# Kernel tuning notes

Hardware: AMD Instinct MI355X
Metric: run time of the kernel (lower is better)

The kernel has to match this reference:

```python
import jax, jax.numpy as jnp
import numpy as np
from jax import lax

B, T, K, HID, NCLS = 32, 2048, 17, 64, 10
DILATIONS = (1, 1, 2)
RESIDUAL = (False, True, True)
TK = 3  # temporal kernel
BN_EPS = 1e-5
LN_EPS = 1e-5

COCO_EDGES = [(0,1),(0,2),(1,3),(2,4),(5,6),(5,7),(7,9),(6,8),(8,10),(5,11),(6,12),(11,13),(13,15),(12,14),(14,16)]

def build_skeleton_adj(num_kpts=K):
    adj = np.eye(num_kpts, dtype=np.float32)
    for i, j in COCO_EDGES:
        adj[i, j] = 1.0
        adj[j, i] = 1.0
    adj = adj + np.eye(num_kpts, dtype=np.float32)
    deg = adj.sum(axis=1, keepdims=True)
    deg[deg == 0] = 1.0
    return adj / deg

def setup_inputs() -> dict:
    key = jax.random.key(0)
    ks = jax.random.split(key, 8)
    kpts = jax.random.normal(ks[0], (B, T, K, 3), dtype=jnp.float32)
    adj = jnp.asarray(build_skeleton_adj(K))
    gcn_w0 = jax.random.normal(ks[1], (3, HID), dtype=jnp.float32) * (1.0 / np.sqrt(3))
    gcn_w1 = jax.random.normal(ks[2], (HID, HID), dtype=jnp.float32) * (1.0 / np.sqrt(HID))
    gcn_w2 = jax.random.normal(ks[3], (HID, HID), dtype=jnp.float32) * (1.0 / np.sqrt(HID))
    tcn_w = jax.random.normal(ks[4], (3, HID, HID, TK, 1), dtype=jnp.float32) * (1.0 / np.sqrt(HID * TK))
    bn_scale = 1.0 + 0.1 * jax.random.normal(ks[5], (3, HID), dtype=jnp.float32)
    bn_bias = 0.1 * jax.random.normal(ks[6], (3, HID), dtype=jnp.float32)
    bn_mean = 0.1 * jax.random.normal(ks[7], (3, HID), dtype=jnp.float32)
    bn_var = 0.5 + jax.random.uniform(jax.random.fold_in(key, 7), (3, HID), dtype=jnp.float32)
    ln_scale = jnp.ones((HID,), dtype=jnp.float32)
    ln_bias = jnp.zeros((HID,), dtype=jnp.float32)
    fc_w = jax.random.normal(jax.random.fold_in(key, 8), (HID, NCLS), dtype=jnp.float32) * (1.0 / np.sqrt(HID))
    fc_b = jnp.zeros((NCLS,), dtype=jnp.float32)
    return dict(kpts=kpts, adj=adj, gcn_w0=gcn_w0, gcn_w1=gcn_w1, gcn_w2=gcn_w2,
                tcn_w=tcn_w, bn_scale=bn_scale, bn_bias=bn_bias, bn_mean=bn_mean,
                bn_var=bn_var, ln_scale=ln_scale, ln_bias=ln_bias, fc_w=fc_w, fc_b=fc_b)

def _stgn_block(x, adj, gw, tw, bs, bb, bm, bv, dilation, residual):
    # x: [B, C_in, T, K]
    y = jnp.einsum('bctk,kv->bctv', x, adj)          # graph conv over keypoints
    y = jnp.einsum('bitk,io->botk', y, gw)           # channel mixing (intended GCN weight)
    pad = (TK - 1) * dilation // 2
    y = lax.conv_general_dilated(y, tw, window_strides=(1, 1),
                                 padding=[(pad, pad), (0, 0)],
                                 rhs_dilation=(dilation, 1),
                                 dimension_numbers=('NCHW', 'OIHW', 'NCHW'))
    inv = (bs / jnp.sqrt(bv + BN_EPS))[None, :, None, None]
    y = y * inv + (bb - bs * bm / jnp.sqrt(bv + BN_EPS))[None, :, None, None]
    y = jax.nn.relu(y)
    if residual:
        y = y + x
    return y

def reference(kpts, adj, gcn_w0, gcn_w1, gcn_w2, tcn_w, bn_scale, bn_bias, bn_mean,
              bn_var, ln_scale, ln_bias, fc_w, fc_b):
    x = jnp.transpose(kpts, (0, 3, 1, 2))  # [B, 3, T, K]
    gws = (gcn_w0, gcn_w1, gcn_w2)
    for i in range(3):
        x = _stgn_block(x, adj, gws[i], tcn_w[i], bn_scale[i], bn_bias[i],
                        bn_mean[i], bn_var[i], DILATIONS[i], RESIDUAL[i])
    feat = x.mean(axis=(2, 3))  # [B, HID] temporal/spatial mean pool
    mu = feat.mean(axis=-1, keepdims=True)
    var = feat.var(axis=-1, keepdims=True)
    feat = (feat - mu) / jnp.sqrt(var + LN_EPS) * ln_scale + ln_bias
    return feat @ fc_w + fc_b  # [B, NCLS]
```

## Files before the change

### kernel.cpp

```cpp
#include <hip/hip_runtime.h>
#include <hip/hip_fp16.h>
#include <math.h>

#define T_DIM 2048
#define TP_DIM 2052
#define K_DIM 17
#define HID   64
#define B_DIM 32

typedef short s16x8 __attribute__((ext_vector_type(8)));
typedef unsigned u32x2 __attribute__((ext_vector_type(2)));
typedef float f32x4 __attribute__((ext_vector_type(4)));
typedef _Float16 f16x2 __attribute__((ext_vector_type(2)));

__device__ __forceinline__ unsigned pkh(float lo, float hi) {
    return __builtin_bit_cast(unsigned, __builtin_amdgcn_cvt_pkrtz(lo, hi));
}
__device__ __forceinline__ f16x2 u2h(unsigned v) {
    return __builtin_bit_cast(f16x2, v);
}
__device__ __forceinline__ unsigned h2u(f16x2 v) {
    return __builtin_bit_cast(unsigned, v);
}
__device__ __forceinline__ short f2h(float f) {
    _Float16 h = (_Float16)f;
    return __builtin_bit_cast(short, h);
}

static constexpr int NBR_PTR[18] = {0,3,6,9,11,13,17,21,24,27,29,31,34,37,40,43,45,47};
static constexpr int NBR_K[47] = {
    0,1,2,  0,1,3,  0,2,4,  1,3,  2,4,
    5,6,7,11,  5,6,8,12,  5,7,9,  6,8,10,  7,9,  8,10,
    5,11,13,  6,12,14,  11,13,15,  12,14,16,  13,15,  14,16 };
__device__ const int d_NBR_PTR[18] = {0,3,6,9,11,13,17,21,24,27,29,31,34,37,40,43,45,47};
__device__ const int d_NBR_K[47] = {
    0,1,2,  0,1,3,  0,2,4,  1,3,  2,4,
    5,6,7,11,  5,6,8,12,  5,7,9,  6,8,10,  7,9,  8,10,
    5,11,13,  6,12,14,  11,13,15,  12,14,16,  13,15,  14,16 };

__global__ void fold_weights_kernel(
    const float* __restrict__ gw0, const float* __restrict__ gw1,
    const float* __restrict__ gw2, const float* __restrict__ tcn,
    const float* __restrict__ bns, const float* __restrict__ bnb,
    const float* __restrict__ bnm, const float* __restrict__ bnv,
    short* __restrict__ effT0, short* __restrict__ effT12,
    float* __restrict__ bnc)
{
    int tid = blockIdx.x * blockDim.x + threadIdx.x;
    int stride = gridDim.x * blockDim.x;
    for (int idx = tid; idx < 2048; idx += stride) {
        int o = idx >> 5, k = idx & 31, dt = k >> 3, cin = k & 7;
        float s = 0.f;
        if (dt < 3 && cin < 3)
            for (int m = 0; m < 64; m++)
                s += gw0[cin * 64 + m] * tcn[(o * 64 + m) * 3 + dt];
        effT0[idx] = f2h(s);
    }
    for (int idx = tid; idx < 24576; idx += stride) {
        int blk = idx / 12288;
        int r = idx - blk * 12288;
        int o = r / 192, k = r - o * 192, dt = k >> 6, c = k & 63;
        const float* gw = blk ? gw2 : gw1;
        const float* tw = tcn + (size_t)(blk + 1) * 64 * 64 * 3;
        float s = 0.f;
        for (int m = 0; m < 64; m++)
            s += gw[c * 64 + m] * tw[(o * 64 + m) * 3 + dt];
        effT12[idx] = f2h(s);
    }
    for (int i = tid; i < 192; i += stride) {
        float inv = bns[i] * rsqrtf(bnv[i] + 1e-5f);
        bnc[i] = inv;
        bnc[192 + i] = bnb[i] - bnm[i] * inv;
    }
}

__global__ __launch_bounds__(256) void premix_kernel(
    const float* __restrict__ x, const float* __restrict__ adj,
    float* __restrict__ xg, short* __restrict__ y2, int cb)
{
    const int idx = blockIdx.x * 256 + threadIdx.x;
    const int total = cb * TP_DIM * K_DIM;
    if (idx < total) {
        const int b = idx / (TP_DIM * K_DIM);
        const int rem = idx - b * (TP_DIM * K_DIM);
        const int tp = rem / K_DIM, j = rem - tp * K_DIM;
        const int t = tp - 2;
        float a0 = 0.f, a1 = 0.f, a2 = 0.f;
        if (t >= 0 && t < T_DIM) {
            const float* xp = x + ((size_t)b * T_DIM + t) * 51;
            const int p0 = d_NBR_PTR[j], p1 = d_NBR_PTR[j + 1];
            for (int e = p0; e < p1; e++) {
                int k = d_NBR_K[e];
                float w = adj[k * 17 + j];
                a0 += w * xp[k * 3 + 0];
                a1 += w * xp[k * 3 + 1];
                a2 += w * xp[k * 3 + 2];
            }
        }
        float* op = xg + ((size_t)b * TP_DIM + tp) * 52 + j * 3;
        op[0] = a0; op[1] = a1; op[2] = a2;
    }
    const int zn = cb * 4 * 1088;
    for (int z = idx; z < zn; z += gridDim.x * 256) {
        int bb = z / (4 * 1088);
        int rr = z - bb * 4 * 1088;
        int pi = rr / 1088;
        int ci = rr - pi * 1088;
        int tp = (pi < 2) ? pi : (2048 + pi);
        y2[((size_t)(bb * TP_DIM + tp) * K_DIM) * 64 + ci] = 0;
    }
}

__global__ __launch_bounds__(256, 4) void stgcn_ab_kernel(
    const float* __restrict__ xg, const float* __restrict__ adj,
    const short* __restrict__ effT0, const short* __restrict__ effT12,
    const float* __restrict__ bnc, short* __restrict__ y2)
{
    __shared__ unsigned adj_h[289];
    __shared__ __align__(16) float xtg[12 * 52];
    __shared__ __align__(16) short ybuf[170 * 72];

    const int tid = threadIdx.x;
    const int b = blockIdx.y;
    const int t0 = blockIdx.x * 8;
    const int lane = tid & 63, wave = tid >> 6;
    const int col = lane & 15, kgrp = lane >> 4;

    for (int i = tid; i < 289; i += 256) {
        float w = adj[i];
        adj_h[i] = pkh(w, w);
    }
    {
        const float4* src = (const float4*)(xg + ((size_t)b * TP_DIM + t0) * 52);
        float4* dst = (float4*)xtg;
        for (int i = tid; i < 156; i += 256) dst[i] = src[i];
    }
    s16x8 af1 = *(const s16x8*)(effT0 + (wave * 16 + col) * 32 + kgrp * 8);
    s16x8 af2[6];
    #pragma unroll
    for (int kk = 0; kk < 6; kk++)
        af2[kk] = *(const s16x8*)(effT12 +
            (wave * 16 + col) * 192 + kk * 32 + kgrp * 8);
    __syncthreads();

    {
        f32x4 inv4 = *(const f32x4*)&bnc[wave * 16 + kgrp * 4];
        f32x4 sh4  = *(const f32x4*)&bnc[192 + wave * 16 + kgrp * 4];
        for (int tile = 0; tile < 11; tile++) {
            const int r = tile * 16 + col;
            const int me = r < 170 ? r : 169;
            const int s = (me * 241) >> 12;
            const int j = me - s * 17;
            int4 bz = {0, 0, 0, 0};
            if (kgrp < 3) {
                const float* xp = &xtg[(s + kgrp) * 52 + j * 3];
                bz.x = (int)pkh(xp[0], xp[1]);
                bz.y = (int)pkh(xp[2], 0.f);
            }
            s16x8 bfr = __builtin_bit_cast(s16x8, bz);
            f32x4 acc = __builtin_amdgcn_mfma_f32_16x16x32_f16(
                af1, bfr, (f32x4){0.f, 0.f, 0.f, 0.f}, 0, 0, 0);
            const int t = t0 - 1 + s;
            const bool valid = (t >= 0) && (t < T_DIM);
            if (r < 170) {
                float v0 = valid ? fmaxf(acc[0] * inv4[0] + sh4[0], 0.f) : 0.f;
                float v1 = valid ? fmaxf(acc[1] * inv4[1] + sh4[1], 0.f) : 0.f;
                float v2 = valid ? fmaxf(acc[2] * inv4[2] + sh4[2], 0.f) : 0.f;
                float v3 = valid ? fmaxf(acc[3] * inv4[3] + sh4[3], 0.f) : 0.f;
                u32x2 st; st[0] = pkh(v0, v1); st[1] = pkh(v2, v3);
                *(u32x2*)&ybuf[r * 72 + wave * 16 + kgrp * 4] = st;
            }
        }
    }
    __syncthreads();

    f32x4 acc2[9];
    #pragma unroll
    for (int t2 = 0; t2 < 9; t2++) acc2[t2] = (f32x4){0.f, 0.f, 0.f, 0.f};
    #pragma unroll
    for (int kk = 0; kk < 6; kk++) {
        #pragma unroll
        for (int t2 = 0; t2 < 9; t2++) {
            const int r = t2 * 16 + col;
            const int me = r < 136 ? r : 135;
            s16x8 bfr = *(const s16x8*)&ybuf[
                (me + 17 * (kk >> 1)) * 72 + (kk & 1) * 32 + kgrp * 8];
            acc2[t2] = __builtin_amdgcn_mfma_f32_16x16x32_f16(
                af2[kk], bfr, acc2[t2], 0, 0, 0);
        }
    }
    unsigned rv[17];
    {
        const int tl = tid >> 5, o0 = (tid & 31) * 2;
        #pragma unroll
        for (int v = 0; v < 17; v++)
            rv[v] = *(const unsigned*)&ybuf[((tl + 1) * 17 + v) * 72 + o0];
    }
    __syncthreads();

    #pragma unroll
    for (int t2 = 0; t2 < 9; t2++) {
        const int r = t2 * 16 + col;
        if (r < 136) {
            u32x2 st;
            st[0] = pkh(acc2[t2][0], acc2[t2][1]);
            st[1] = pkh(acc2[t2][2], acc2[t2][3]);
            *(u32x2*)&ybuf[r * 72 + wave * 16 + kgrp * 4] = st;
        }
    }
    __syncthreads();

    {
        const int tl = tid >> 5, o0 = (tid & 31) * 2;
        const f16x2 inv2 = u2h(pkh(bnc[64 + o0], bnc[64 + o0 + 1]));
        const f16x2 sh2  = u2h(pkh(bnc[256 + o0], bnc[256 + o0 + 1]));
        const f16x2 zero = u2h(0u);
        f16x2 zk[17];
        #pragma unroll
        for (int k = 0; k < 17; k++)
            zk[k] = u2h(*(const unsigned*)&ybuf[(tl * 17 + k) * 72 + o0]);
        const size_t gout = ((size_t)b * TP_DIM + t0 + tl + 2) * K_DIM * 64;
        #pragma unroll
        for (int v = 0; v < 17; v++) {
            f16x2 g = zero;
            #pragma unroll
            for (int e = NBR_PTR[v]; e < NBR_PTR[v + 1]; e++) {
                int k = NBR_K[e];
                g = u2h(adj_h[k * 17 + v]) * zk[k] + g;
            }
            f16x2 val = __builtin_elementwise_max(g * inv2 + sh2, zero);
            val = val + u2h(rv[v]);
            *(unsigned*)&y2[gout + (size_t)v * 64 + o0] = h2u(val);
        }
    }
}

__global__ __launch_bounds__(256, 4) void stgcn_c_kernel(
    const short* __restrict__ y2, const float* __restrict__ adj,
    const short* __restrict__ effW3, const float* __restrict__ bnc,
    float* __restrict__ part, int b0)
{
    __shared__ unsigned adj_h[289];
    __shared__ __align__(16) short ybuf[204 * 72];

    float* pr = (float*)&ybuf[136 * 72];

    const int tid = threadIdx.x;
    const int b = blockIdx.y;
    const int t0 = blockIdx.x * 8;
    const int lane = tid & 63, wave = tid >> 6;
    const int col = lane & 15, kgrp = lane >> 4;

    for (int i = tid; i < 289; i += 256) {
        float w = adj[i];
        adj_h[i] = pkh(w, w);
    }
    s16x8 af3[6];
    #pragma unroll
    for (int kk = 0; kk < 6; kk++)
        af3[kk] = *(const s16x8*)(effW3 +
            (wave * 16 + col) * 192 + kk * 32 + kgrp * 8);

    {
        const short* base = y2 + ((size_t)b * TP_DIM + t0) * K_DIM * 64;
        for (int idx = tid; idx < 1632; idx += 256) {
            const int row = idx >> 3, c = idx & 7;
            *(s16x8*)&ybuf[row * 72 + c * 8] =
                *(const s16x8*)(base + (size_t)row * 64 + c * 8);
        }
    }
    __syncthreads();

    f32x4 acc3[9];
    #pragma unroll
    for (int t3 = 0; t3 < 9; t3++) acc3[t3] = (f32x4){0.f, 0.f, 0.f, 0.f};
    #pragma unroll
    for (int kk = 0; kk < 6; kk++) {
        #pragma unroll
        for (int t3 = 0; t3 < 9; t3++) {
            const int r = t3 * 16 + col;
            const int me = r < 136 ? r : 135;
            s16x8 bfr = *(const s16x8*)&ybuf[
                (me + 34 * (kk >> 1)) * 72 + (kk & 1) * 32 + kgrp * 8];
            acc3[t3] = __builtin_amdgcn_mfma_f32_16x16x32_f16(
                af3[kk], bfr, acc3[t3], 0, 0, 0);
        }
    }
    f16x2 rs = u2h(0u);
    {
        const int tl = tid >> 5, o0 = (tid & 31) * 2;
        #pragma unroll
        for (int v = 0; v < 17; v++)
            rs = rs + u2h(*(const unsigned*)&ybuf[((tl + 2) * 17 + v) * 72 + o0]);
    }
    __syncthreads();

    #pragma unroll
    for (int t3 = 0; t3 < 9; t3++) {
        const int r = t3 * 16 + col;
        if (r < 136) {
            u32x2 st;
            st[0] = pkh(acc3[t3][0], acc3[t3][1]);
            st[1] = pkh(acc3[t3][2], acc3[t3][3]);
            *(u32x2*)&ybuf[r * 72 + wave * 16 + kgrp * 4] = st;
        }
    }
    __syncthreads();

    {
        const int tl = tid >> 5, o0 = (tid & 31) * 2;
        const f16x2 inv2 = u2h(pkh(bnc[128 + o0], bnc[128 + o0 + 1]));
        const f16x2 sh2  = u2h(pkh(bnc[320 + o0], bnc[320 + o0 + 1]));
        const f16x2 zero = u2h(0u);
        f16x2 zk[17];
        #pragma unroll
        for (int k = 0; k < 17; k++)
            zk[k] = u2h(*(const unsigned*)&ybuf[(tl * 17 + k) * 72 + o0]);
        float ps0 = (float)rs[0], ps1 = (float)rs[1];
        #pragma unroll
        for (int v = 0; v < 17; v++) {
            f16x2 g = zero;
            #pragma unroll
            for (int e = NBR_PTR[v]; e < NBR_PTR[v + 1]; e++) {
                int k = NBR_K[e];
                g = u2h(adj_h[k * 17 + v]) * zk[k] + g;
            }
            f16x2 val = __builtin_elementwise_max(g * inv2 + sh2, zero);
            ps0 += (float)val[0];
            ps1 += (float)val[1];
        }
        *(float2*)&pr[tl * 64 + o0] = make_float2(ps0, ps1);
    }
    __syncthreads();
    if (tid < 64) {
        float s = 0.f;
        #pragma unroll
        for (int i = 0; i < 8; i++) s += pr[i * 64 + tid];
        part[((size_t)(b0 + b) * 256 + blockIdx.x) * 64 + tid] = s;
    }
}

__global__ __launch_bounds__(256) void finish_kernel(
    const float* __restrict__ part, const float* __restrict__ ln_s,
    const float* __restrict__ ln_b, const float* __restrict__ fc_w,
    const float* __restrict__ fc_b, float* __restrict__ out)
{
    __shared__ float red[4][64];
    __shared__ float ns[64];
    const int b = blockIdx.x;
    const int g = threadIdx.x >> 6, c = threadIdx.x & 63;
    float s = 0.f;
    for (int j = 0; j < 64; j++)
        s += part[((size_t)b * 256 + g * 64 + j) * 64 + c];
    red[g][c] = s;
    __syncthreads();
    if (threadIdx.x < 64) {
        float feat = (red[0][c] + red[1][c] + red[2][c] + red[3][c])
                   / (float)(T_DIM * K_DIM);
        float m = feat;
        #pragma unroll
        for (int off = 32; off > 0; off >>= 1) m += __shfl_down(m, off);
        m = __shfl(m, 0) / 64.f;
        float d = feat - m;
        float v = d * d;
        #pragma unroll
        for (int off = 32; off > 0; off >>= 1) v += __shfl_down(v, off);
        v = __shfl(v, 0) / 64.f;
        ns[c] = d * rsqrtf(v + 1e-5f) * ln_s[c] + ln_b[c];
    }
    __syncthreads();
    if (threadIdx.x < 10) {
        float o = fc_b[threadIdx.x];
        for (int i = 0; i < 64; i++) o += ns[i] * fc_w[i * 10 + threadIdx.x];
        out[b * 10 + threadIdx.x] = o;
    }
}

extern "C" void kernel_launch(void* const* d_in, const int* in_sizes, int n_in,
                              void* d_out, int out_size, void* d_ws, size_t ws_size,
                              hipStream_t stream)
{
    const float* kpts = (const float*)d_in[0];
    const float* adj  = (const float*)d_in[1];
    const float* gw0  = (const float*)d_in[2];
    const float* gw1  = (const float*)d_in[3];
    const float* gw2  = (const float*)d_in[4];
    const float* tcn  = (const float*)d_in[5];
    const float* bns  = (const float*)d_in[6];
    const float* bnb  = (const float*)d_in[7];
    const float* bnm  = (const float*)d_in[8];
    const float* bnv  = (const float*)d_in[9];
    const float* lns  = (const float*)d_in[10];
    const float* lnb  = (const float*)d_in[11];
    const float* fcw  = (const float*)d_in[12];
    const float* fcb  = (const float*)d_in[13];
    float* out = (float*)d_out;

    float* bnc  = (float*)d_ws;
    float* part = bnc + 384;
    short* effT0  = (short*)(part + (size_t)B_DIM * 256 * 64);
    short* effT12 = effT0 + 2048;
    float* xg     = (float*)(effT12 + 24576);
    const size_t fixed_bytes = 384 * 4 + (size_t)B_DIM * 256 * 64 * 4
                             + 2048 * 2 + 24576 * 2;
    const size_t xg_per_b = (size_t)TP_DIM * 52 * 4;
    const size_t y2_per_b = (size_t)TP_DIM * K_DIM * 64 * 2;

    int cb = B_DIM;
    while (cb > 1 &&
           fixed_bytes + (size_t)cb * (xg_per_b + y2_per_b) > ws_size)
        cb >>= 1;
    short* y2 = (short*)(xg + (size_t)cb * TP_DIM * 52);

    fold_weights_kernel<<<64, 256, 0, stream>>>(gw0, gw1, gw2, tcn,
                                                bns, bnb, bnm, bnv,
                                                effT0, effT12, bnc);

    const int pm_blocks = (cb * TP_DIM * K_DIM + 255) / 256;
    for (int b0 = 0; b0 < B_DIM; b0 += cb) {
        premix_kernel<<<pm_blocks, 256, 0, stream>>>(
            kpts + (size_t)b0 * T_DIM * K_DIM * 3, adj, xg, y2, cb);
        stgcn_ab_kernel<<<dim3(T_DIM / 8, cb), 256, 0, stream>>>(
            xg, adj, effT0, effT12, bnc, y2);
        stgcn_c_kernel<<<dim3(T_DIM / 8, cb), 256, 0, stream>>>(
            y2, adj, effT12 + 12288, bnc, part, b0);
    }

    finish_kernel<<<B_DIM, 256, 0, stream>>>(part, lns, lnb, fcw, fcb, out);
}
```

Measured before the change: 227.3 us.

## Move block-3 graph mix into ab kernel and pool residual there

```diff
diff --git a/kernel.cpp b/kernel.cpp
--- a/kernel.cpp
+++ b/kernel.cpp
@@ -76,7 +76,7 @@
 
 __global__ __launch_bounds__(256) void premix_kernel(
     const float* __restrict__ x, const float* __restrict__ adj,
-    float* __restrict__ xg, short* __restrict__ y2, int cb)
+    float* __restrict__ xg, short* __restrict__ y2g, int cb)
 {
     const int idx = blockIdx.x * 256 + threadIdx.x;
     const int total = cb * TP_DIM * K_DIM;
@@ -107,18 +107,21 @@
         int pi = rr / 1088;
         int ci = rr - pi * 1088;
         int tp = (pi < 2) ? pi : (2048 + pi);
-        y2[((size_t)(bb * TP_DIM + tp) * K_DIM) * 64 + ci] = 0;
+        y2g[((size_t)(bb * TP_DIM + tp) * K_DIM) * 64 + ci] = 0;
     }
 }
 
 __global__ __launch_bounds__(256, 4) void stgcn_ab_kernel(
     const float* __restrict__ xg, const float* __restrict__ adj,
     const short* __restrict__ effT0, const short* __restrict__ effT12,
-    const float* __restrict__ bnc, short* __restrict__ y2)
+    const float* __restrict__ bnc, short* __restrict__ y2g,
+    float* __restrict__ part2, int b0)
 {
     __shared__ unsigned adj_h[289];
     __shared__ __align__(16) float xtg[12 * 52];
     __shared__ __align__(16) short ybuf[170 * 72];
+
+    float* pr = (float*)&ybuf[136 * 72];
 
     const int tid = threadIdx.x;
     const int b = blockIdx.y;
@@ -219,7 +222,8 @@
         #pragma unroll
         for (int k = 0; k < 17; k++)
             zk[k] = u2h(*(const unsigned*)&ybuf[(tl * 17 + k) * 72 + o0]);
-        const size_t gout = ((size_t)b * TP_DIM + t0 + tl + 2) * K_DIM * 64;
+        f16x2 y2v[17];
+        f16x2 pool = zero;
         #pragma unroll
         for (int v = 0; v < 17; v++) {
             f16x2 g = zero;
@@ -230,20 +234,38 @@
             }
             f16x2 val = __builtin_elementwise_max(g * inv2 + sh2, zero);
             val = val + u2h(rv[v]);
-            *(unsigned*)&y2[gout + (size_t)v * 64 + o0] = h2u(val);
-        }
-    }
-}
-
-__global__ __launch_bounds__(256, 4) void stgcn_c_kernel(
-    const short* __restrict__ y2, const float* __restrict__ adj,
-    const short* __restrict__ effW3, const float* __restrict__ bnc,
-    float* __restrict__ part, int b0)
-{
-    __shared__ unsigned adj_h[289];
+            y2v[v] = val;
+            pool = pool + val;
+        }
+        const size_t gout = ((size_t)b * TP_DIM + t0 + tl + 2) * K_DIM * 64;
+        #pragma unroll
+        for (int j = 0; j < 17; j++) {
+            f16x2 gg = zero;
+            #pragma unroll
+            for (int e = NBR_PTR[j]; e < NBR_PTR[j + 1]; e++) {
+                int k = NBR_K[e];
+                gg = u2h(adj_h[k * 17 + j]) * y2v[k] + gg;
+            }
+            *(unsigned*)&y2g[gout + (size_t)j * 64 + o0] = h2u(gg);
+        }
+        pr[tl * 64 + o0]     = (float)pool[0];
+        pr[tl * 64 + o0 + 1] = (float)pool[1];
+    }
+    __syncthreads();
+    if (tid < 64) {
+        float s = 0.f;
+        #pragma unroll
+        for (int i = 0; i < 8; i++) s += pr[i * 64 + tid];
+        part2[((size_t)(b0 + b) * 256 + blockIdx.x) * 64 + tid] = s;
+    }
+}
+
+__global__ __launch_bounds__(256, 5) void stgcn_c_kernel(
+    const short* __restrict__ y2g, const short* __restrict__ effW3,
+    const float* __restrict__ bnc, float* __restrict__ part, int b0)
+{
     __shared__ __align__(16) short ybuf[204 * 72];
-
-    float* pr = (float*)&ybuf[136 * 72];
+    __shared__ float pr[64];
 
     const int tid = threadIdx.x;
     const int b = blockIdx.y;
@@ -251,18 +273,16 @@
     const int lane = tid & 63, wave = tid >> 6;
     const int col = lane & 15, kgrp = lane >> 4;
 
-    for (int i = tid; i < 289; i += 256) {
-        float w = adj[i];
-        adj_h[i] = pkh(w, w);
-    }
     s16x8 af3[6];
     #pragma unroll
     for (int kk = 0; kk < 6; kk++)
         af3[kk] = *(const s16x8*)(effW3 +
             (wave * 16 + col) * 192 + kk * 32 + kgrp * 8);
+    const f32x4 inv4 = *(const f32x4*)&bnc[128 + wave * 16 + kgrp * 4];
+    const f32x4 sh4  = *(const f32x4*)&bnc[320 + wave * 16 + kgrp * 4];
 
     {
-        const short* base = y2 + ((size_t)b * TP_DIM + t0) * K_DIM * 64;
+        const short* base = y2g + ((size_t)b * TP_DIM + t0) * K_DIM * 64;
         for (int idx = tid; idx < 1632; idx += 256) {
             const int row = idx >> 3, c = idx & 7;
             *(s16x8*)&ybuf[row * 72 + c * 8] =
@@ -271,87 +291,54 @@
     }
     __syncthreads();
 
-    f32x4 acc3[9];
-    #pragma unroll
-    for (int t3 = 0; t3 < 9; t3++) acc3[t3] = (f32x4){0.f, 0.f, 0.f, 0.f};
-    #pragma unroll
-    for (int kk = 0; kk < 6; kk++) {
-        #pragma unroll
-        for (int t3 = 0; t3 < 9; t3++) {
-            const int r = t3 * 16 + col;
-            const int me = r < 136 ? r : 135;
+    float psum[4] = {0.f, 0.f, 0.f, 0.f};
+    for (int t3 = 0; t3 < 9; t3++) {
+        const int r = t3 * 16 + col;
+        const int me = r < 136 ? r : 135;
+        f32x4 acc = (f32x4){0.f, 0.f, 0.f, 0.f};
+        #pragma unroll
+        for (int kk = 0; kk < 6; kk++) {
             s16x8 bfr = *(const s16x8*)&ybuf[
                 (me + 34 * (kk >> 1)) * 72 + (kk & 1) * 32 + kgrp * 8];
-            acc3[t3] = __builtin_amdgcn_mfma_f32_16x16x32_f16(
-                af3[kk], bfr, acc3[t3], 0, 0, 0);
-        }
-    }
-    f16x2 rs = u2h(0u);
-    {
-        const int tl = tid >> 5, o0 = (tid & 31) * 2;
-        #pragma unroll
-        for (int v = 0; v < 17; v++)
-            rs = rs + u2h(*(const unsigned*)&ybuf[((tl + 2) * 17 + v) * 72 + o0]);
-    }
-    __syncthreads();
-
-    #pragma unroll
-    for (int t3 = 0; t3 < 9; t3++) {
-        const int r = t3 * 16 + col;
+            acc = __builtin_amdgcn_mfma_f32_16x16x32_f16(af3[kk], bfr, acc, 0, 0, 0);
+        }
         if (r < 136) {
-            u32x2 st;
-            st[0] = pkh(acc3[t3][0], acc3[t3][1]);
-            st[1] = pkh(acc3[t3][2], acc3[t3][3]);
-            *(u32x2*)&ybuf[r * 72 + wave * 16 + kgrp * 4] = st;
-        }
-    }
-    __syncthreads();
-
-    {
-        const int tl = tid >> 5, o0 = (tid & 31) * 2;
-        const f16x2 inv2 = u2h(pkh(bnc[128 + o0], bnc[128 + o0 + 1]));
-        const f16x2 sh2  = u2h(pkh(bnc[320 + o0], bnc[320 + o0 + 1]));
-        const f16x2 zero = u2h(0u);
-        f16x2 zk[17];
-        #pragma unroll
-        for (int k = 0; k < 17; k++)
-            zk[k] = u2h(*(const unsigned*)&ybuf[(tl * 17 + k) * 72 + o0]);
-        float ps0 = (float)rs[0], ps1 = (float)rs[1];
-        #pragma unroll
-        for (int v = 0; v < 17; v++) {
-            f16x2 g = zero;
-            #pragma unroll
-            for (int e = NBR_PTR[v]; e < NBR_PTR[v + 1]; e++) {
-                int k = NBR_K[e];
-                g = u2h(adj_h[k * 17 + v]) * zk[k] + g;
-            }
-            f16x2 val = __builtin_elementwise_max(g * inv2 + sh2, zero);
-            ps0 += (float)val[0];
-            ps1 += (float)val[1];
-        }
-        *(float2*)&pr[tl * 64 + o0] = make_float2(ps0, ps1);
-    }
-    __syncthreads();
-    if (tid < 64) {
-        float s = 0.f;
-        #pragma unroll
-        for (int i = 0; i < 8; i++) s += pr[i * 64 + tid];
-        part[((size_t)(b0 + b) * 256 + blockIdx.x) * 64 + tid] = s;
-    }
+            psum[0] += fmaxf(acc[0] * inv4[0] + sh4[0], 0.f);
+            psum[1] += fmaxf(acc[1] * inv4[1] + sh4[1], 0.f);
+            psum[2] += fmaxf(acc[2] * inv4[2] + sh4[2], 0.f);
+            psum[3] += fmaxf(acc[3] * inv4[3] + sh4[3], 0.f);
+        }
+    }
+    #pragma unroll
+    for (int off = 1; off <= 8; off <<= 1) {
+        psum[0] += __shfl_xor(psum[0], off);
+        psum[1] += __shfl_xor(psum[1], off);
+        psum[2] += __shfl_xor(psum[2], off);
+        psum[3] += __shfl_xor(psum[3], off);
+    }
+    if (col == 0)
+        *(f32x4*)&pr[wave * 16 + kgrp * 4] =
+            (f32x4){psum[0], psum[1], psum[2], psum[3]};
+    __syncthreads();
+    if (tid < 64)
+        part[((size_t)(b0 + b) * 256 + blockIdx.x) * 64 + tid] = pr[tid];
 }
 
 __global__ __launch_bounds__(256) void finish_kernel(
-    const float* __restrict__ part, const float* __restrict__ ln_s,
-    const float* __restrict__ ln_b, const float* __restrict__ fc_w,
-    const float* __restrict__ fc_b, float* __restrict__ out)
+    const float* __restrict__ part, const float* __restrict__ part2,
+    const float* __restrict__ ln_s, const float* __restrict__ ln_b,
+    const float* __restrict__ fc_w, const float* __restrict__ fc_b,
+    float* __restrict__ out)
 {
     __shared__ float red[4][64];
     __shared__ float ns[64];
     const int b = blockIdx.x;
     const int g = threadIdx.x >> 6, c = threadIdx.x & 63;
     float s = 0.f;
-    for (int j = 0; j < 64; j++)
-        s += part[((size_t)b * 256 + g * 64 + j) * 64 + c];
+    for (int j = 0; j < 64; j++) {
+        size_t i = ((size_t)b * 256 + g * 64 + j) * 64 + c;
+        s += part[i] + part2[i];
+    }
     red[g][c] = s;
     __syncthreads();
     if (threadIdx.x < 64) {
@@ -396,21 +383,22 @@
     const float* fcb  = (const float*)d_in[13];
     float* out = (float*)d_out;
 
-    float* bnc  = (float*)d_ws;
-    float* part = bnc + 384;
-    short* effT0  = (short*)(part + (size_t)B_DIM * 256 * 64);
+    float* bnc   = (float*)d_ws;
+    float* part  = bnc + 384;
+    float* part2 = part + (size_t)B_DIM * 256 * 64;
+    short* effT0  = (short*)(part2 + (size_t)B_DIM * 256 * 64);
     short* effT12 = effT0 + 2048;
     float* xg     = (float*)(effT12 + 24576);
-    const size_t fixed_bytes = 384 * 4 + (size_t)B_DIM * 256 * 64 * 4
+    const size_t fixed_bytes = 384 * 4 + 2 * (size_t)B_DIM * 256 * 64 * 4
                              + 2048 * 2 + 24576 * 2;
-    const size_t xg_per_b = (size_t)TP_DIM * 52 * 4;
-    const size_t y2_per_b = (size_t)TP_DIM * K_DIM * 64 * 2;
+    const size_t xg_per_b  = (size_t)TP_DIM * 52 * 4;
+    const size_t y2g_per_b = (size_t)TP_DIM * K_DIM * 64 * 2;
 
     int cb = B_DIM;
     while (cb > 1 &&
-           fixed_bytes + (size_t)cb * (xg_per_b + y2_per_b) > ws_size)
+           fixed_bytes + (size_t)cb * (xg_per_b + y2g_per_b) > ws_size)
         cb >>= 1;
-    short* y2 = (short*)(xg + (size_t)cb * TP_DIM * 52);
+    short* y2g = (short*)(xg + (size_t)cb * TP_DIM * 52);
 
     fold_weights_kernel<<<64, 256, 0, stream>>>(gw0, gw1, gw2, tcn,
                                                 bns, bnb, bnm, bnv,
@@ -419,12 +407,13 @@
     const int pm_blocks = (cb * TP_DIM * K_DIM + 255) / 256;
     for (int b0 = 0; b0 < B_DIM; b0 += cb) {
         premix_kernel<<<pm_blocks, 256, 0, stream>>>(
-            kpts + (size_t)b0 * T_DIM * K_DIM * 3, adj, xg, y2, cb);
+            kpts + (size_t)b0 * T_DIM * K_DIM * 3, adj, xg, y2g, cb);
         stgcn_ab_kernel<<<dim3(T_DIM / 8, cb), 256, 0, stream>>>(
-            xg, adj, effT0, effT12, bnc, y2);
+            xg, adj, effT0, effT12, bnc, y2g, part2, b0);
         stgcn_c_kernel<<<dim3(T_DIM / 8, cb), 256, 0, stream>>>(
-            y2, adj, effT12 + 12288, bnc, part, b0);
-    }
-
-    finish_kernel<<<B_DIM, 256, 0, stream>>>(part, lns, lnb, fcw, fcb, out);
-}
+            y2g, effT12 + 12288, bnc, part, b0);
+    }
+
+    finish_kernel<<<B_DIM, 256, 0, stream>>>(part, part2, lns, lnb,
+                                             fcw, fcb, out);
+}
```

Result: no change. 230.0 us (+1.2%).
